# Performance work log

Hardware: AMD Instinct MI355X
Metric: run time of the kernel (lower is better)

## Reference

```python
import jax, jax.numpy as jnp
import numpy as np

L, H, D_IN, D_OUT = 2, 768, 768, 512


def _gru_layer(x, w_ih, w_hh, b_ih, b_hh):
    # x: [B,T,D]; w_ih: [3H,D]; w_hh: [3H,H]; b_ih,b_hh: [3H]
    # PyTorch GRU gate order: r, z, n
    gates_x = jnp.einsum('btd,gd->btg', x, w_ih) + b_ih  # [B,T,3H], precomputed once
    gates_x = jnp.swapaxes(gates_x, 0, 1)  # [T,B,3H] for scan over time
    h0 = jnp.zeros((x.shape[0], w_hh.shape[1]), dtype=x.dtype)

    def step(h, gx):
        gh = h @ w_hh.T + b_hh  # [B,3H]
        xr, xz, xn = jnp.split(gx, 3, axis=-1)
        hr, hz, hn = jnp.split(gh, 3, axis=-1)
        r = jax.nn.sigmoid(xr + hr)
        z = jax.nn.sigmoid(xz + hz)
        n = jnp.tanh(xn + r * hn)
        h_new = (1.0 - z) * n + z * h
        return h_new, h_new

    _, ys = jax.lax.scan(step, h0, gates_x)  # ys: [T,B,H]
    return jnp.swapaxes(ys, 0, 1)  # [B,T,H]


def setup_inputs() -> dict:
    key = jax.random.key(0)
    ks = jax.random.split(key, 6)
    B, T = 16, 1024
    s = 1.0 / np.sqrt(H)  # PyTorch RNN init scale
    x = jax.random.normal(ks[0], (B, T, D_IN), dtype=jnp.float32)
    # stacked per-layer GRU weights (D_IN == H so layer 0 stacks cleanly)
    w_ih = jax.random.uniform(ks[1], (L, 3 * H, H), minval=-s, maxval=s, dtype=jnp.float32)
    w_hh = jax.random.uniform(ks[2], (L, 3 * H, H), minval=-s, maxval=s, dtype=jnp.float32)
    b_ih = jax.random.uniform(ks[3], (L, 3 * H), minval=-s, maxval=s, dtype=jnp.float32)
    b_hh = jax.random.uniform(ks[4], (L, 3 * H), minval=-s, maxval=s, dtype=jnp.float32)
    w_fc = jax.random.normal(ks[5], (D_OUT, H), dtype=jnp.float32) * 0.02
    b_fc = jnp.zeros((D_OUT,), dtype=jnp.float32)
    return {"x": x, "w_ih": w_ih, "w_hh": w_hh, "b_ih": b_ih, "b_hh": b_hh,
            "w_fc": w_fc, "b_fc": b_fc}


def reference(x, w_ih, w_hh, b_ih, b_hh, w_fc, b_fc):
    out = x
    for l in range(L):  # small fixed layer loop
        out = _gru_layer(out, w_ih[l], w_hh[l], b_ih[l], b_hh[l])
    out = jnp.einsum('bth,oh->bto', out, w_fc) + b_fc  # Linear(768->512)
    return jax.nn.gelu(out, approximate=False)  # torch gelu (exact)
```

## Files before the change

kernel.cpp:

```cpp
#include <hip/hip_runtime.h>
#include <hip/hip_bf16.h>

#define H     768
#define G3    2304
#define BATCH 16
#define TLEN  1024
#define DOUT  512
#define SLICE 32
#define WPG   24
#define NWG   96
#define NTHR  384

typedef __attribute__((ext_vector_type(8))) short short8;
typedef __attribute__((ext_vector_type(4))) float f32x4;
typedef __attribute__((ext_vector_type(4))) unsigned int u32x4;

union U8 { short8 s; unsigned u[4]; unsigned long long q[2]; };

__device__ __forceinline__ float b2f(ushort u) {
  union { unsigned int ui; float f; } v; v.ui = ((unsigned int)u) << 16; return v.f;
}
__device__ __forceinline__ ushort f2b(float f) {
  union { float f; unsigned int ui; } v; v.f = f;
  unsigned int u = v.ui;
  return (ushort)((u + 0x7fffu + ((u >> 16) & 1u)) >> 16);
}

__device__ __forceinline__ unsigned long long agent_ld64(const void* p) {
  return __hip_atomic_load((const unsigned long long*)p, __ATOMIC_RELAXED, __HIP_MEMORY_SCOPE_AGENT);
}
__device__ __forceinline__ unsigned agent_ld32(const void* p) {
  return __hip_atomic_load((const unsigned*)p, __ATOMIC_RELAXED, __HIP_MEMORY_SCOPE_AGENT);
}
__device__ __forceinline__ void agent_st32(void* p, unsigned v) {
  __hip_atomic_store((unsigned*)p, v, __ATOMIC_RELAXED, __HIP_MEMORY_SCOPE_AGENT);
}
__device__ __forceinline__ void agent_st64(void* p, unsigned long long v) {
  __hip_atomic_store((unsigned long long*)p, v, __ATOMIC_RELAXED, __HIP_MEMORY_SCOPE_AGENT);
}

__device__ __forceinline__ void ld64B_agent(const void* p, u32x4* r) {
  asm volatile(
    "global_load_dwordx4 %0, %4, off sc0 sc1\n\t"
    "global_load_dwordx4 %1, %4, off offset:16 sc0 sc1\n\t"
    "global_load_dwordx4 %2, %4, off offset:32 sc0 sc1\n\t"
    "global_load_dwordx4 %3, %4, off offset:48 sc0 sc1\n\t"
    "s_waitcnt vmcnt(0)"
    : "=&v"(r[0]), "=&v"(r[1]), "=&v"(r[2]), "=&v"(r[3])
    : "v"(p) : "memory");
}

__device__ __forceinline__ short8 loadA8(const void* base, bool bf, size_t eidx) {
  if (bf) return *(const short8*)((const ushort*)base + eidx);
  const uint4* f = (const uint4*)((const float*)base + eidx);
  uint4 lo = f[0];
  uint4 hi = f[1];
  U8 r;
  r.u[0] = __builtin_amdgcn_perm(lo.y, lo.x, 0x07060302);
  r.u[1] = __builtin_amdgcn_perm(lo.w, lo.z, 0x07060302);
  r.u[2] = __builtin_amdgcn_perm(hi.y, hi.x, 0x07060302);
  r.u[3] = __builtin_amdgcn_perm(hi.w, hi.z, 0x07060302);
  return r.s;
}
__device__ __forceinline__ short8 loadW8(const void* base, bool bf, size_t eidx) {
  if (bf) return *(const short8*)((const ushort*)base + eidx);
  const float* f = (const float*)base + eidx;
  short8 r;
  #pragma unroll
  for (int i = 0; i < 8; i++) r[i] = (short)f2b(f[i]);
  return r;
}
__device__ __forceinline__ float loadS(const void* p, bool bf, size_t i) {
  return bf ? b2f(((const ushort*)p)[i]) : ((const float*)p)[i];
}

__device__ __forceinline__ bool detect_bf16(const unsigned* xw, int tid, int nthr, int* sh) {
  if (tid == 0) *sh = 0;
  __syncthreads();
  int c = 0;
  for (int i = tid; i < 4096; i += nthr) {
    int e = (int)((xw[i] >> 7) & 0xFF);
    c += (e >= 110 && e <= 140) ? 1 : 0;
  }
  atomicAdd(sh, c);
  __syncthreads();
  return *sh > 2048;
}

__device__ __forceinline__ unsigned* flagp(unsigned* flags, int grp, int wgi, int rep) {
  return flags + (((grp * WPG + wgi) * 4 + rep) * 32);
}

__global__ __launch_bounds__(NTHR) void scan_kernel(
    const void* __restrict__ x,
    const void* __restrict__ w_ih,
    const void* __restrict__ w_hh,
    const void* __restrict__ b_ih,
    const void* __restrict__ b_hh,
    unsigned int* flags,
    unsigned int* dflag,
    ushort* h1buf,
    float*  gxbuf1,
    float*  gxbuf2,
    ushort* y2)
{
  const int wg   = blockIdx.x;
  const int grp  = wg / WPG;
  const int wgi  = wg % WPG;
  const int tid  = threadIdx.x;
  const int wave = tid >> 6;
  const int lane = tid & 63;
  const int quad = lane >> 4;
  const bool isL = (grp == 1 || grp == 3);

  __shared__ ushort h_lds[BATCH * H];
  __shared__ float ghs[96 * 17];
  __shared__ float hold[BATCH * SLICE];
  __shared__ float bih_s[96], bhh_s[96];
  __shared__ int   detsh;

  const bool isbf = detect_bf16((const unsigned*)x, tid, NTHR, &detsh);
  if (tid == 0) dflag[0] = isbf ? 1u : 0u;

  for (int i = tid; i < BATCH * SLICE; i += NTHR) hold[i] = 0.0f;

  if (isL) {
    size_t boff = (grp == 3) ? (size_t)G3 : 0;
    for (int gf = tid; gf < 96; gf += NTHR) {
      size_t gidx = boff + (size_t)(gf >> 5) * H + wgi * SLICE + (gf & 31);
      bih_s[gf] = loadS(b_ih, isbf, gidx);
      bhh_s[gf] = loadS(b_hh, isbf, gidx);
    }
  }

  const unsigned* pollp = nullptr;
  int polloff = 0;
  if (wave == 0) {
    if (grp == 0) {
      if (lane == 0) { pollp = flagp(flags, 1, wgi, 2); polloff = -2; }
    } else if (grp == 1) {
      if      (lane == 0)  { pollp = flagp(flags, 0, wgi, 0);       polloff = 0;  }
      else if (lane <= 24) { pollp = flagp(flags, 1, lane - 1, 0);  polloff = 0;  }
      else if (lane <= 48) { pollp = flagp(flags, 2, lane - 25, 0); polloff = -2; }
    } else if (grp == 2) {
      if      (lane < 24)  { pollp = flagp(flags, 1, lane, 1);      polloff = 0;  }
      else if (lane == 24) { pollp = flagp(flags, 3, wgi, 1);       polloff = -1; }
    } else {
      if      (lane == 0)  { pollp = flagp(flags, 2, wgi, 1);       polloff = -1; }
      else if (lane <= 24) { pollp = flagp(flags, 3, lane - 1, 0);  polloff = 0;  }
    }
  }

  const void* Wmat = (grp == 0 || grp == 2) ? w_ih : w_hh;
  const size_t woff = (grp >= 2) ? (size_t)G3 * H : 0;
  const int gate   = wave >> 1;
  const int gfbase = gate * SLICE + (wave & 1) * 16;
  const int nrow   = gate * H + wgi * SLICE + (wave & 1) * 16 + (lane & 15);
  const size_t wbase = woff + (size_t)nrow * H + quad * 8;

  short8 bfrag[24];
  #pragma unroll
  for (int kk = 0; kk < 24; kk++)
    bfrag[kk] = loadW8(Wmat, isbf, wbase + kk * 32);

  const int sb  = tid / 24;
  const int seg = tid % 24;
  const int sx  = sb & 7;

  const int pb = tid >> 4;
  const int pj = (tid & 15) * 2;
  const bool pact = isL && (tid < BATCH * SLICE / 2);

  const int lag = (grp == 1) ? 1 : ((grp == 2) ? 2 : ((grp == 3) ? 4 : 0));

  __syncthreads();

  for (int t = 0; t < TLEN + 4; t++) {
    const int tau = t - lag;
    const bool active = (tau >= 0) && (tau < TLEN);

    if (active) {
      if (wave == 0) {
        for (;;) {
          int v = pollp ? (int)agent_ld32(pollp) : 0x7FFFFFFF;
          if (__ballot(v < t + polloff) == 0ull) break;
          __builtin_amdgcn_s_sleep(1);
        }
      }
      __syncthreads();

      unsigned long long gr01 = 0, gz01 = 0, gn01 = 0;
      if (pact) {
        const float* gxr = ((grp == 1) ? gxbuf1 : gxbuf2)
            + ((size_t)((tau & 3) * WPG + wgi) * BATCH + pb) * 96;
        gr01 = agent_ld64(gxr + pj);
        gz01 = agent_ld64(gxr + 32 + pj);
        gn01 = agent_ld64(gxr + 64 + pj);
      }

      if (grp == 0) {
        const size_t srcbase = ((size_t)sb * TLEN + tau) * H + seg * 32;
        #pragma unroll
        for (int i = 0; i < 4; i++) {
          short8 v = loadA8(x, isbf, srcbase + i * 8);
          *(short8*)&h_lds[sb * H + (((seg * 4 + i) ^ sx) * 8)] = v;
        }
      } else {
        const int hstep = (grp == 3) ? (t - 5) : (t - 2);
        u32x4 r4[4];
        if (hstep >= 0) {
          const ushort* src = (grp == 3)
              ? y2 + ((size_t)sb * TLEN + hstep) * H + seg * 32
              : h1buf + (size_t)(hstep & 3) * (BATCH * H) + (size_t)sb * H + seg * 32;
          ld64B_agent(src, r4);
        } else {
          r4[0] = (u32x4){0u, 0u, 0u, 0u};
          r4[1] = r4[0]; r4[2] = r4[0]; r4[3] = r4[0];
        }
        #pragma unroll
        for (int j = 0; j < 4; j++)
          *(u32x4*)&h_lds[sb * H + (((seg * 4 + j) ^ sx) * 8)] = r4[j];
      }
      __syncthreads();

      const int ar  = lane & 15;
      const int arx = ar & 7;
      const ushort* abase = &h_lds[ar * H];
      f32x4 acc0 = {0.f, 0.f, 0.f, 0.f}, acc1 = {0.f, 0.f, 0.f, 0.f};
      #pragma unroll
      for (int kk = 0; kk < 12; kk++) {
        short8 a0 = *(const short8*)&abase[((quad + 4 * kk) ^ arx) * 8];
        short8 a1 = *(const short8*)&abase[((quad + 4 * (kk + 12)) ^ arx) * 8];
        acc0 = __builtin_amdgcn_mfma_f32_16x16x32_bf16(a0, bfrag[kk],      acc0, 0, 0, 0);
        acc1 = __builtin_amdgcn_mfma_f32_16x16x32_bf16(a1, bfrag[kk + 12], acc1, 0, 0, 0);
      }
      f32x4 acc = acc0 + acc1;

      #pragma unroll
      for (int i = 0; i < 4; i++)
        ghs[(gfbase + (lane & 15)) * 17 + quad * 4 + i] = acc[i];
      __syncthreads();

      if (!isL) {
        float* gxout = ((grp == 0) ? gxbuf1 : gxbuf2)
            + ((size_t)(tau & 3) * WPG + wgi) * BATCH * 96;
        const int m  = tid / 24;
        const int c4 = (tid % 24) * 4;
        union { unsigned long long q; float f[2]; } p0, p1;
        p0.f[0] = ghs[(c4 + 0) * 17 + m];
        p0.f[1] = ghs[(c4 + 1) * 17 + m];
        p1.f[0] = ghs[(c4 + 2) * 17 + m];
        p1.f[1] = ghs[(c4 + 3) * 17 + m];
        agent_st64(gxout + (size_t)m * 96 + c4,     p0.q);
        agent_st64(gxout + (size_t)m * 96 + c4 + 2, p1.q);
      } else if (pact) {
        union { unsigned long long q; float f[2]; } ur, uz, un;
        ur.q = gr01; uz.q = gz01; un.q = gn01;
        unsigned hpack = 0;
        #pragma unroll
        for (int s = 0; s < 2; s++) {
          const int j = pj + s;
          float rpre = ur.f[s] + bih_s[j]      + ghs[j * 17 + pb]        + bhh_s[j];
          float zpre = uz.f[s] + bih_s[32 + j] + ghs[(32 + j) * 17 + pb] + bhh_s[32 + j];
          float hn   = ghs[(64 + j) * 17 + pb] + bhh_s[64 + j];
          float r = 1.0f / (1.0f + expf(-rpre));
          float z = 1.0f / (1.0f + expf(-zpre));
          float n = tanhf(un.f[s] + bih_s[64 + j] + r * hn);
          float hnew = (1.0f - z) * n + z * hold[pb * SLICE + j];
          hold[pb * SLICE + j] = hnew;
          hpack |= ((unsigned)f2b(hnew)) << (16 * s);
        }
        if (grp == 1)
          agent_st32(h1buf + (size_t)(tau & 3) * (BATCH * H)
                           + (size_t)pb * H + wgi * SLICE + pj, hpack);
        else
          agent_st32(&y2[((size_t)pb * TLEN + tau) * H + wgi * SLICE + pj], hpack);
      }
    }

    __syncthreads();
    if (tid < 4) agent_st32(flagp(flags, grp, wgi, tid), (unsigned)(t + 1));
  }
}

__global__ __launch_bounds__(256) void fc_kernel(
    const ushort* __restrict__ y2,
    const void* __restrict__ w_fc,
    const void* __restrict__ b_fc,
    const unsigned* __restrict__ dflag,
    void* __restrict__ out)
{
  const bool isbf = dflag[0] != 0u;
  const int wave = threadIdx.x >> 6;
  const int lane = threadIdx.x & 63;
  const int col  = lane & 15;
  const int quad = lane >> 4;
  const int m0 = blockIdx.x * 64 + wave * 16;
  const int n0 = blockIdx.y * 64;

  const ushort* arow = y2 + (size_t)(m0 + col) * H + quad * 8;
  const size_t bbase = (size_t)(n0 + col) * H + quad * 8;

  f32x4 acc[4];
  #pragma unroll
  for (int nt = 0; nt < 4; nt++) acc[nt] = (f32x4){0.f, 0.f, 0.f, 0.f};

  for (int kk = 0; kk < 24; kk++) {
    short8 a = *(const short8*)(arow + kk * 32);
    #pragma unroll
    for (int nt = 0; nt < 4; nt++) {
      short8 b = loadA8(w_fc, isbf, bbase + (size_t)nt * 16 * H + kk * 32);
      acc[nt] = __builtin_amdgcn_mfma_f32_16x16x32_bf16(a, b, acc[nt], 0, 0, 0);
    }
  }

  #pragma unroll
  for (int nt = 0; nt < 4; nt++) {
    #pragma unroll
    for (int i = 0; i < 4; i++) {
      int m = m0 + quad * 4 + i;
      int n = n0 + nt * 16 + col;
      float v = acc[nt][i] + loadS(b_fc, isbf, n);
      float g = 0.5f * v * (1.0f + erff(v * 0.70710678118654752f));
      if (isbf) ((ushort*)out)[(size_t)m * DOUT + n] = f2b(g);
      else      ((float*)out)[(size_t)m * DOUT + n] = g;
    }
  }
}

extern "C" void kernel_launch(void* const* d_in, const int* in_sizes, int n_in,
                              void* d_out, int out_size, void* d_ws, size_t ws_size,
                              hipStream_t stream) {
  const void* x    = d_in[0];
  const void* w_ih = d_in[1];
  const void* w_hh = d_in[2];
  const void* b_ih = d_in[3];
  const void* b_hh = d_in[4];
  const void* w_fc = d_in[5];
  const void* b_fc = d_in[6];

  char* ws = (char*)d_ws;
  unsigned int* flags = (unsigned int*)(ws);
  unsigned int* dflag = (unsigned int*)(ws + 49152);
  ushort* h1buf  = (ushort*)(ws + 53248);
  float*  gxbuf1 = (float*)(ws + 151552);
  float*  gxbuf2 = (float*)(ws + 741376);
  ushort* y2     = (ushort*)(ws + 1331200);

  hipMemsetAsync(ws, 0, 49156, stream);
  scan_kernel<<<dim3(NWG), dim3(NTHR), 0, stream>>>(
      x, w_ih, w_hh, b_ih, b_hh, flags, dflag,
      h1buf, gxbuf1, gxbuf2, y2);
  fc_kernel<<<dim3(16384 / 64, DOUT / 64), dim3(256), 0, stream>>>(
      y2, w_fc, b_fc, dflag, (void*)d_out);
}
```

Measured before the change: 3.676 ms.

## Merge layer-2 input projection into layer-1 recurrent group, cutting workgroups to 72

```diff
diff --git a/kernel.cpp b/kernel.cpp
--- a/kernel.cpp
+++ b/kernel.cpp
@@ -8,7 +8,7 @@
 #define DOUT  512
 #define SLICE 32
 #define WPG   24
-#define NWG   96
+#define NWG   72
 #define NTHR  384
 
 typedef __attribute__((ext_vector_type(8))) short short8;
@@ -48,6 +48,13 @@
     "s_waitcnt vmcnt(0)"
     : "=&v"(r[0]), "=&v"(r[1]), "=&v"(r[2]), "=&v"(r[3])
     : "v"(p) : "memory");
+}
+
+__device__ __forceinline__ float fsigmoid(float x) {
+  return 1.0f / (1.0f + __expf(-x));
+}
+__device__ __forceinline__ float ftanh(float x) {
+  return 1.0f - 2.0f / (__expf(2.0f * x) + 1.0f);
 }
 
 __device__ __forceinline__ short8 loadA8(const void* base, bool bf, size_t eidx) {
@@ -91,7 +98,7 @@
   return flags + (((grp * WPG + wgi) * 4 + rep) * 32);
 }
 
-__global__ __launch_bounds__(NTHR) void scan_kernel(
+__global__ __launch_bounds__(NTHR, 1) void scan_kernel(
     const void* __restrict__ x,
     const void* __restrict__ w_ih,
     const void* __restrict__ w_hh,
@@ -111,10 +118,10 @@
   const int wave = tid >> 6;
   const int lane = tid & 63;
   const int quad = lane >> 4;
-  const bool isL = (grp == 1 || grp == 3);
 
   __shared__ ushort h_lds[BATCH * H];
   __shared__ float ghs[96 * 17];
+  __shared__ float ghs2[96 * 17];
   __shared__ float hold[BATCH * SLICE];
   __shared__ float bih_s[96], bhh_s[96];
   __shared__ int   detsh;
@@ -124,8 +131,8 @@
 
   for (int i = tid; i < BATCH * SLICE; i += NTHR) hold[i] = 0.0f;
 
-  if (isL) {
-    size_t boff = (grp == 3) ? (size_t)G3 : 0;
+  if (grp >= 1) {
+    size_t boff = (grp == 2) ? (size_t)G3 : 0;
     for (int gf = tid; gf < 96; gf += NTHR) {
       size_t gidx = boff + (size_t)(gf >> 5) * H + wgi * SLICE + (gf & 31);
       bih_s[gf] = loadS(b_ih, isbf, gidx);
@@ -139,29 +146,33 @@
     if (grp == 0) {
       if (lane == 0) { pollp = flagp(flags, 1, wgi, 2); polloff = -2; }
     } else if (grp == 1) {
-      if      (lane == 0)  { pollp = flagp(flags, 0, wgi, 0);       polloff = 0;  }
-      else if (lane <= 24) { pollp = flagp(flags, 1, lane - 1, 0);  polloff = 0;  }
-      else if (lane <= 48) { pollp = flagp(flags, 2, lane - 25, 0); polloff = -2; }
-    } else if (grp == 2) {
-      if      (lane < 24)  { pollp = flagp(flags, 1, lane, 1);      polloff = 0;  }
-      else if (lane == 24) { pollp = flagp(flags, 3, wgi, 1);       polloff = -1; }
+      if      (lane == 0)  { pollp = flagp(flags, 0, wgi, 0);      polloff = 0;  }
+      else if (lane <= 24) { pollp = flagp(flags, 1, lane - 1, 0); polloff = 0;  }
+      else if (lane == 25) { pollp = flagp(flags, 2, wgi, 1);      polloff = -1; }
     } else {
-      if      (lane == 0)  { pollp = flagp(flags, 2, wgi, 1);       polloff = -1; }
-      else if (lane <= 24) { pollp = flagp(flags, 3, lane - 1, 0);  polloff = 0;  }
+      if      (lane == 0)  { pollp = flagp(flags, 1, wgi, 1);      polloff = -1; }
+      else if (lane <= 24) { pollp = flagp(flags, 2, lane - 1, 0); polloff = 0;  }
     }
   }
 
-  const void* Wmat = (grp == 0 || grp == 2) ? w_ih : w_hh;
-  const size_t woff = (grp >= 2) ? (size_t)G3 * H : 0;
+  const void* WmatA = (grp == 0) ? w_ih : w_hh;
+  const size_t woffA = (grp == 2) ? (size_t)G3 * H : 0;
   const int gate   = wave >> 1;
   const int gfbase = gate * SLICE + (wave & 1) * 16;
   const int nrow   = gate * H + wgi * SLICE + (wave & 1) * 16 + (lane & 15);
-  const size_t wbase = woff + (size_t)nrow * H + quad * 8;
+  const size_t wrow = (size_t)nrow * H + quad * 8;
 
   short8 bfrag[24];
   #pragma unroll
   for (int kk = 0; kk < 24; kk++)
-    bfrag[kk] = loadW8(Wmat, isbf, wbase + kk * 32);
+    bfrag[kk] = loadW8(WmatA, isbf, woffA + wrow + kk * 32);
+
+  short8 bfrag2[24];
+  if (grp == 1) {
+    #pragma unroll
+    for (int kk = 0; kk < 24; kk++)
+      bfrag2[kk] = loadW8(w_ih, isbf, (size_t)G3 * H + wrow + kk * 32);
+  }
 
   const int sb  = tid / 24;
   const int seg = tid % 24;
@@ -169,15 +180,17 @@
 
   const int pb = tid >> 4;
   const int pj = (tid & 15) * 2;
-  const bool pact = isL && (tid < BATCH * SLICE / 2);
-
-  const int lag = (grp == 1) ? 1 : ((grp == 2) ? 2 : ((grp == 3) ? 4 : 0));
+  const bool pact = (grp >= 1) && (tid < BATCH * SLICE / 2);
+
+  const int lag = (grp == 1) ? 1 : ((grp == 2) ? 4 : 0);
 
   __syncthreads();
 
   for (int t = 0; t < TLEN + 4; t++) {
     const int tau = t - lag;
-    const bool active = (tau >= 0) && (tau < TLEN);
+    const bool act_h = (tau >= 0) && (tau < TLEN);
+    const bool act_g = (grp == 1) && (t >= 2) && (t - 2 < TLEN);
+    const bool active = act_h || act_g;
 
     if (active) {
       if (wave == 0) {
@@ -190,7 +203,7 @@
       __syncthreads();
 
       unsigned long long gr01 = 0, gz01 = 0, gn01 = 0;
-      if (pact) {
+      if (pact && act_h) {
         const float* gxr = ((grp == 1) ? gxbuf1 : gxbuf2)
             + ((size_t)((tau & 3) * WPG + wgi) * BATCH + pb) * 96;
         gr01 = agent_ld64(gxr + pj);
@@ -206,10 +219,10 @@
           *(short8*)&h_lds[sb * H + (((seg * 4 + i) ^ sx) * 8)] = v;
         }
       } else {
-        const int hstep = (grp == 3) ? (t - 5) : (t - 2);
+        const int hstep = (grp == 1) ? (t - 2) : (t - 5);
         u32x4 r4[4];
         if (hstep >= 0) {
-          const ushort* src = (grp == 3)
+          const ushort* src = (grp == 2)
               ? y2 + ((size_t)sb * TLEN + hstep) * H + seg * 32
               : h1buf + (size_t)(hstep & 3) * (BATCH * H) + (size_t)sb * H + seg * 32;
           ld64B_agent(src, r4);
@@ -227,23 +240,41 @@
       const int arx = ar & 7;
       const ushort* abase = &h_lds[ar * H];
       f32x4 acc0 = {0.f, 0.f, 0.f, 0.f}, acc1 = {0.f, 0.f, 0.f, 0.f};
-      #pragma unroll
-      for (int kk = 0; kk < 12; kk++) {
-        short8 a0 = *(const short8*)&abase[((quad + 4 * kk) ^ arx) * 8];
-        short8 a1 = *(const short8*)&abase[((quad + 4 * (kk + 12)) ^ arx) * 8];
-        acc0 = __builtin_amdgcn_mfma_f32_16x16x32_bf16(a0, bfrag[kk],      acc0, 0, 0, 0);
-        acc1 = __builtin_amdgcn_mfma_f32_16x16x32_bf16(a1, bfrag[kk + 12], acc1, 0, 0, 0);
-      }
-      f32x4 acc = acc0 + acc1;
+      f32x4 acc2 = {0.f, 0.f, 0.f, 0.f}, acc3 = {0.f, 0.f, 0.f, 0.f};
+      if (grp == 1) {
+        #pragma unroll
+        for (int kk = 0; kk < 12; kk++) {
+          short8 a0 = *(const short8*)&abase[((quad + 4 * kk) ^ arx) * 8];
+          short8 a1 = *(const short8*)&abase[((quad + 4 * (kk + 12)) ^ arx) * 8];
+          acc0 = __builtin_amdgcn_mfma_f32_16x16x32_bf16(a0, bfrag[kk],       acc0, 0, 0, 0);
+          acc1 = __builtin_amdgcn_mfma_f32_16x16x32_bf16(a1, bfrag[kk + 12],  acc1, 0, 0, 0);
+          acc2 = __builtin_amdgcn_mfma_f32_16x16x32_bf16(a0, bfrag2[kk],      acc2, 0, 0, 0);
+          acc3 = __builtin_amdgcn_mfma_f32_16x16x32_bf16(a1, bfrag2[kk + 12], acc3, 0, 0, 0);
+        }
+      } else {
+        #pragma unroll
+        for (int kk = 0; kk < 12; kk++) {
+          short8 a0 = *(const short8*)&abase[((quad + 4 * kk) ^ arx) * 8];
+          short8 a1 = *(const short8*)&abase[((quad + 4 * (kk + 12)) ^ arx) * 8];
+          acc0 = __builtin_amdgcn_mfma_f32_16x16x32_bf16(a0, bfrag[kk],      acc0, 0, 0, 0);
+          acc1 = __builtin_amdgcn_mfma_f32_16x16x32_bf16(a1, bfrag[kk + 12], acc1, 0, 0, 0);
+        }
+      }
+      f32x4 accA = acc0 + acc1;
 
       #pragma unroll
       for (int i = 0; i < 4; i++)
-        ghs[(gfbase + (lane & 15)) * 17 + quad * 4 + i] = acc[i];
+        ghs[(gfbase + ar) * 17 + quad * 4 + i] = accA[i];
+      if (grp == 1) {
+        f32x4 accB = acc2 + acc3;
+        #pragma unroll
+        for (int i = 0; i < 4; i++)
+          ghs2[(gfbase + ar) * 17 + quad * 4 + i] = accB[i];
+      }
       __syncthreads();
 
-      if (!isL) {
-        float* gxout = ((grp == 0) ? gxbuf1 : gxbuf2)
-            + ((size_t)(tau & 3) * WPG + wgi) * BATCH * 96;
+      if (grp == 0) {
+        float* gxout = gxbuf1 + ((size_t)(tau & 3) * WPG + wgi) * BATCH * 96;
         const int m  = tid / 24;
         const int c4 = (tid % 24) * 4;
         union { unsigned long long q; float f[2]; } p0, p1;
@@ -253,33 +284,47 @@
         p1.f[1] = ghs[(c4 + 3) * 17 + m];
         agent_st64(gxout + (size_t)m * 96 + c4,     p0.q);
         agent_st64(gxout + (size_t)m * 96 + c4 + 2, p1.q);
-      } else if (pact) {
-        union { unsigned long long q; float f[2]; } ur, uz, un;
-        ur.q = gr01; uz.q = gz01; un.q = gn01;
-        unsigned hpack = 0;
-        #pragma unroll
-        for (int s = 0; s < 2; s++) {
-          const int j = pj + s;
-          float rpre = ur.f[s] + bih_s[j]      + ghs[j * 17 + pb]        + bhh_s[j];
-          float zpre = uz.f[s] + bih_s[32 + j] + ghs[(32 + j) * 17 + pb] + bhh_s[32 + j];
-          float hn   = ghs[(64 + j) * 17 + pb] + bhh_s[64 + j];
-          float r = 1.0f / (1.0f + expf(-rpre));
-          float z = 1.0f / (1.0f + expf(-zpre));
-          float n = tanhf(un.f[s] + bih_s[64 + j] + r * hn);
-          float hnew = (1.0f - z) * n + z * hold[pb * SLICE + j];
-          hold[pb * SLICE + j] = hnew;
-          hpack |= ((unsigned)f2b(hnew)) << (16 * s);
-        }
-        if (grp == 1)
-          agent_st32(h1buf + (size_t)(tau & 3) * (BATCH * H)
-                           + (size_t)pb * H + wgi * SLICE + pj, hpack);
-        else
-          agent_st32(&y2[((size_t)pb * TLEN + tau) * H + wgi * SLICE + pj], hpack);
+      } else {
+        if (act_g) {
+          float* gxout = gxbuf2 + ((size_t)((t - 2) & 3) * WPG + wgi) * BATCH * 96;
+          const int m  = tid / 24;
+          const int c4 = (tid % 24) * 4;
+          union { unsigned long long q; float f[2]; } p0, p1;
+          p0.f[0] = ghs2[(c4 + 0) * 17 + m];
+          p0.f[1] = ghs2[(c4 + 1) * 17 + m];
+          p1.f[0] = ghs2[(c4 + 2) * 17 + m];
+          p1.f[1] = ghs2[(c4 + 3) * 17 + m];
+          agent_st64(gxout + (size_t)m * 96 + c4,     p0.q);
+          agent_st64(gxout + (size_t)m * 96 + c4 + 2, p1.q);
+        }
+        if (act_h && pact) {
+          union { unsigned long long q; float f[2]; } ur, uz, un;
+          ur.q = gr01; uz.q = gz01; un.q = gn01;
+          unsigned hpack = 0;
+          #pragma unroll
+          for (int s = 0; s < 2; s++) {
+            const int j = pj + s;
+            float rpre = ur.f[s] + bih_s[j]      + ghs[j * 17 + pb]        + bhh_s[j];
+            float zpre = uz.f[s] + bih_s[32 + j] + ghs[(32 + j) * 17 + pb] + bhh_s[32 + j];
+            float hn   = ghs[(64 + j) * 17 + pb] + bhh_s[64 + j];
+            float r = fsigmoid(rpre);
+            float z = fsigmoid(zpre);
+            float n = ftanh(un.f[s] + bih_s[64 + j] + r * hn);
+            float hnew = (1.0f - z) * n + z * hold[pb * SLICE + j];
+            hold[pb * SLICE + j] = hnew;
+            hpack |= ((unsigned)f2b(hnew)) << (16 * s);
+          }
+          if (grp == 1)
+            agent_st32(h1buf + (size_t)(tau & 3) * (BATCH * H)
+                             + (size_t)pb * H + wgi * SLICE + pj, hpack);
+          else
+            agent_st32(&y2[((size_t)pb * TLEN + tau) * H + wgi * SLICE + pj], hpack);
+        }
       }
     }
 
     __syncthreads();
-    if (tid < 4) agent_st32(flagp(flags, grp, wgi, tid), (unsigned)(t + 1));
+    if (tid < 3) agent_st32(flagp(flags, grp, wgi, tid), (unsigned)(t + 1));
   }
 }
 
```

Result: slower. 5.007 ms (+36.2%).

## Halve scan workgroup count by widening each workgroup to 64 gate columns

Applied to the files above, without the earlier changes.

```diff
diff --git a/kernel.cpp b/kernel.cpp
--- a/kernel.cpp
+++ b/kernel.cpp
@@ -6,10 +6,10 @@
 #define BATCH 16
 #define TLEN  1024
 #define DOUT  512
-#define SLICE 32
-#define WPG   24
-#define NWG   96
-#define NTHR  384
+#define GCOL  64
+#define WPG   12
+#define NWG   48
+#define NTHR  768
 
 typedef __attribute__((ext_vector_type(8))) short short8;
 typedef __attribute__((ext_vector_type(4))) float f32x4;
@@ -39,14 +39,12 @@
   __hip_atomic_store((unsigned long long*)p, v, __ATOMIC_RELAXED, __HIP_MEMORY_SCOPE_AGENT);
 }
 
-__device__ __forceinline__ void ld64B_agent(const void* p, u32x4* r) {
+__device__ __forceinline__ void ld32B_agent(const void* p, u32x4* r) {
   asm volatile(
-    "global_load_dwordx4 %0, %4, off sc0 sc1\n\t"
-    "global_load_dwordx4 %1, %4, off offset:16 sc0 sc1\n\t"
-    "global_load_dwordx4 %2, %4, off offset:32 sc0 sc1\n\t"
-    "global_load_dwordx4 %3, %4, off offset:48 sc0 sc1\n\t"
+    "global_load_dwordx4 %0, %2, off sc0 sc1\n\t"
+    "global_load_dwordx4 %1, %2, off offset:16 sc0 sc1\n\t"
     "s_waitcnt vmcnt(0)"
-    : "=&v"(r[0]), "=&v"(r[1]), "=&v"(r[2]), "=&v"(r[3])
+    : "=&v"(r[0]), "=&v"(r[1])
     : "v"(p) : "memory");
 }
 
@@ -114,20 +112,20 @@
   const bool isL = (grp == 1 || grp == 3);
 
   __shared__ ushort h_lds[BATCH * H];
-  __shared__ float ghs[96 * 17];
-  __shared__ float hold[BATCH * SLICE];
-  __shared__ float bih_s[96], bhh_s[96];
+  __shared__ float ghs[192 * 17];
+  __shared__ float hold[BATCH * GCOL];
+  __shared__ float bih_s[192], bhh_s[192];
   __shared__ int   detsh;
 
   const bool isbf = detect_bf16((const unsigned*)x, tid, NTHR, &detsh);
   if (tid == 0) dflag[0] = isbf ? 1u : 0u;
 
-  for (int i = tid; i < BATCH * SLICE; i += NTHR) hold[i] = 0.0f;
+  for (int i = tid; i < BATCH * GCOL; i += NTHR) hold[i] = 0.0f;
 
   if (isL) {
     size_t boff = (grp == 3) ? (size_t)G3 : 0;
-    for (int gf = tid; gf < 96; gf += NTHR) {
-      size_t gidx = boff + (size_t)(gf >> 5) * H + wgi * SLICE + (gf & 31);
+    for (int gf = tid; gf < 192; gf += NTHR) {
+      size_t gidx = boff + (size_t)(gf >> 6) * H + wgi * GCOL + (gf & 63);
       bih_s[gf] = loadS(b_ih, isbf, gidx);
       bhh_s[gf] = loadS(b_hh, isbf, gidx);
     }
@@ -140,22 +138,23 @@
       if (lane == 0) { pollp = flagp(flags, 1, wgi, 2); polloff = -2; }
     } else if (grp == 1) {
       if      (lane == 0)  { pollp = flagp(flags, 0, wgi, 0);       polloff = 0;  }
-      else if (lane <= 24) { pollp = flagp(flags, 1, lane - 1, 0);  polloff = 0;  }
-      else if (lane <= 48) { pollp = flagp(flags, 2, lane - 25, 0); polloff = -2; }
+      else if (lane <= 12) { pollp = flagp(flags, 1, lane - 1, 0);  polloff = 0;  }
+      else if (lane <= 24) { pollp = flagp(flags, 2, lane - 13, 0); polloff = -2; }
     } else if (grp == 2) {
-      if      (lane < 24)  { pollp = flagp(flags, 1, lane, 1);      polloff = 0;  }
-      else if (lane == 24) { pollp = flagp(flags, 3, wgi, 1);       polloff = -1; }
+      if      (lane < 12)  { pollp = flagp(flags, 1, lane, 1);      polloff = 0;  }
+      else if (lane == 12) { pollp = flagp(flags, 3, wgi, 1);       polloff = -1; }
     } else {
       if      (lane == 0)  { pollp = flagp(flags, 2, wgi, 1);       polloff = -1; }
-      else if (lane <= 24) { pollp = flagp(flags, 3, lane - 1, 0);  polloff = 0;  }
+      else if (lane <= 12) { pollp = flagp(flags, 3, lane - 1, 0);  polloff = 0;  }
     }
   }
 
   const void* Wmat = (grp == 0 || grp == 2) ? w_ih : w_hh;
   const size_t woff = (grp >= 2) ? (size_t)G3 * H : 0;
-  const int gate   = wave >> 1;
-  const int gfbase = gate * SLICE + (wave & 1) * 16;
-  const int nrow   = gate * H + wgi * SLICE + (wave & 1) * 16 + (lane & 15);
+  const int gate   = wave >> 2;
+  const int wchunk = wave & 3;
+  const int gfbase = gate * GCOL + wchunk * 16;
+  const int nrow   = gate * H + wgi * GCOL + wchunk * 16 + (lane & 15);
   const size_t wbase = woff + (size_t)nrow * H + quad * 8;
 
   short8 bfrag[24];
@@ -163,13 +162,13 @@
   for (int kk = 0; kk < 24; kk++)
     bfrag[kk] = loadW8(Wmat, isbf, wbase + kk * 32);
 
-  const int sb  = tid / 24;
-  const int seg = tid % 24;
+  const int sb  = tid / 48;
+  const int seg = tid % 48;
   const int sx  = sb & 7;
 
-  const int pb = tid >> 4;
-  const int pj = (tid & 15) * 2;
-  const bool pact = isL && (tid < BATCH * SLICE / 2);
+  const int pb = tid >> 5;
+  const int pj = (tid & 31) * 2;
+  const bool pact = isL && (tid < BATCH * GCOL / 2);
 
   const int lag = (grp == 1) ? 1 : ((grp == 2) ? 2 : ((grp == 3) ? 4 : 0));
 
@@ -192,34 +191,34 @@
       unsigned long long gr01 = 0, gz01 = 0, gn01 = 0;
       if (pact) {
         const float* gxr = ((grp == 1) ? gxbuf1 : gxbuf2)
-            + ((size_t)((tau & 3) * WPG + wgi) * BATCH + pb) * 96;
+            + ((size_t)((tau & 3) * WPG + wgi) * BATCH + pb) * 192;
         gr01 = agent_ld64(gxr + pj);
-        gz01 = agent_ld64(gxr + 32 + pj);
-        gn01 = agent_ld64(gxr + 64 + pj);
+        gz01 = agent_ld64(gxr + 64 + pj);
+        gn01 = agent_ld64(gxr + 128 + pj);
       }
 
       if (grp == 0) {
-        const size_t srcbase = ((size_t)sb * TLEN + tau) * H + seg * 32;
-        #pragma unroll
-        for (int i = 0; i < 4; i++) {
-          short8 v = loadA8(x, isbf, srcbase + i * 8);
-          *(short8*)&h_lds[sb * H + (((seg * 4 + i) ^ sx) * 8)] = v;
-        }
+        const size_t srcbase = ((size_t)sb * TLEN + tau) * H + seg * 16;
+        short8 v0 = loadA8(x, isbf, srcbase);
+        short8 v1 = loadA8(x, isbf, srcbase + 8);
+        const int u0 = seg * 2, u1 = seg * 2 + 1;
+        *(short8*)&h_lds[sb * H + (((u0 & ~7) | ((u0 & 7) ^ sx)) * 8)] = v0;
+        *(short8*)&h_lds[sb * H + (((u1 & ~7) | ((u1 & 7) ^ sx)) * 8)] = v1;
       } else {
         const int hstep = (grp == 3) ? (t - 5) : (t - 2);
-        u32x4 r4[4];
+        u32x4 r4[2];
         if (hstep >= 0) {
           const ushort* src = (grp == 3)
-              ? y2 + ((size_t)sb * TLEN + hstep) * H + seg * 32
-              : h1buf + (size_t)(hstep & 3) * (BATCH * H) + (size_t)sb * H + seg * 32;
-          ld64B_agent(src, r4);
+              ? y2 + ((size_t)sb * TLEN + hstep) * H + seg * 16
+              : h1buf + (size_t)(hstep & 3) * (BATCH * H) + (size_t)sb * H + seg * 16;
+          ld32B_agent(src, r4);
         } else {
           r4[0] = (u32x4){0u, 0u, 0u, 0u};
-          r4[1] = r4[0]; r4[2] = r4[0]; r4[3] = r4[0];
+          r4[1] = r4[0];
         }
-        #pragma unroll
-        for (int j = 0; j < 4; j++)
-          *(u32x4*)&h_lds[sb * H + (((seg * 4 + j) ^ sx) * 8)] = r4[j];
+        const int u0 = seg * 2, u1 = seg * 2 + 1;
+        *(u32x4*)&h_lds[sb * H + (((u0 & ~7) | ((u0 & 7) ^ sx)) * 8)] = r4[0];
+        *(u32x4*)&h_lds[sb * H + (((u1 & ~7) | ((u1 & 7) ^ sx)) * 8)] = r4[1];
       }
       __syncthreads();
 
@@ -229,8 +228,10 @@
       f32x4 acc0 = {0.f, 0.f, 0.f, 0.f}, acc1 = {0.f, 0.f, 0.f, 0.f};
       #pragma unroll
       for (int kk = 0; kk < 12; kk++) {
-        short8 a0 = *(const short8*)&abase[((quad + 4 * kk) ^ arx) * 8];
-        short8 a1 = *(const short8*)&abase[((quad + 4 * (kk + 12)) ^ arx) * 8];
+        const int ua = quad + 4 * kk;
+        const int ub = quad + 4 * (kk + 12);
+        short8 a0 = *(const short8*)&abase[(((ua & ~7) | ((ua & 7) ^ arx)) * 8)];
+        short8 a1 = *(const short8*)&abase[(((ub & ~7) | ((ub & 7) ^ arx)) * 8)];
         acc0 = __builtin_amdgcn_mfma_f32_16x16x32_bf16(a0, bfrag[kk],      acc0, 0, 0, 0);
         acc1 = __builtin_amdgcn_mfma_f32_16x16x32_bf16(a1, bfrag[kk + 12], acc1, 0, 0, 0);
       }
@@ -238,21 +239,21 @@
 
       #pragma unroll
       for (int i = 0; i < 4; i++)
-        ghs[(gfbase + (lane & 15)) * 17 + quad * 4 + i] = acc[i];
+        ghs[(gfbase + ar) * 17 + quad * 4 + i] = acc[i];
       __syncthreads();
 
       if (!isL) {
         float* gxout = ((grp == 0) ? gxbuf1 : gxbuf2)
-            + ((size_t)(tau & 3) * WPG + wgi) * BATCH * 96;
-        const int m  = tid / 24;
-        const int c4 = (tid % 24) * 4;
+            + ((size_t)(tau & 3) * WPG + wgi) * BATCH * 192;
+        const int m  = tid / 48;
+        const int c4 = (tid % 48) * 4;
         union { unsigned long long q; float f[2]; } p0, p1;
         p0.f[0] = ghs[(c4 + 0) * 17 + m];
         p0.f[1] = ghs[(c4 + 1) * 17 + m];
         p1.f[0] = ghs[(c4 + 2) * 17 + m];
         p1.f[1] = ghs[(c4 + 3) * 17 + m];
-        agent_st64(gxout + (size_t)m * 96 + c4,     p0.q);
-        agent_st64(gxout + (size_t)m * 96 + c4 + 2, p1.q);
+        agent_st64(gxout + (size_t)m * 192 + c4,     p0.q);
+        agent_st64(gxout + (size_t)m * 192 + c4 + 2, p1.q);
       } else if (pact) {
         union { unsigned long long q; float f[2]; } ur, uz, un;
         ur.q = gr01; uz.q = gz01; un.q = gn01;
@@ -260,26 +261,26 @@
         #pragma unroll
         for (int s = 0; s < 2; s++) {
           const int j = pj + s;
-          float rpre = ur.f[s] + bih_s[j]      + ghs[j * 17 + pb]        + bhh_s[j];
-          float zpre = uz.f[s] + bih_s[32 + j] + ghs[(32 + j) * 17 + pb] + bhh_s[32 + j];
-          float hn   = ghs[(64 + j) * 17 + pb] + bhh_s[64 + j];
+          float rpre = ur.f[s] + bih_s[j]       + ghs[j * 17 + pb]         + bhh_s[j];
+          float zpre = uz.f[s] + bih_s[64 + j]  + ghs[(64 + j) * 17 + pb]  + bhh_s[64 + j];
+          float hn   = ghs[(128 + j) * 17 + pb] + bhh_s[128 + j];
           float r = 1.0f / (1.0f + expf(-rpre));
           float z = 1.0f / (1.0f + expf(-zpre));
-          float n = tanhf(un.f[s] + bih_s[64 + j] + r * hn);
-          float hnew = (1.0f - z) * n + z * hold[pb * SLICE + j];
-          hold[pb * SLICE + j] = hnew;
+          float n = tanhf(un.f[s] + bih_s[128 + j] + r * hn);
+          float hnew = (1.0f - z) * n + z * hold[pb * GCOL + j];
+          hold[pb * GCOL + j] = hnew;
           hpack |= ((unsigned)f2b(hnew)) << (16 * s);
         }
         if (grp == 1)
           agent_st32(h1buf + (size_t)(tau & 3) * (BATCH * H)
-                           + (size_t)pb * H + wgi * SLICE + pj, hpack);
+                           + (size_t)pb * H + wgi * GCOL + pj, hpack);
         else
-          agent_st32(&y2[((size_t)pb * TLEN + tau) * H + wgi * SLICE + pj], hpack);
+          agent_st32(&y2[((size_t)pb * TLEN + tau) * H + wgi * GCOL + pj], hpack);
       }
     }
 
     __syncthreads();
-    if (tid < 4) agent_st32(flagp(flags, grp, wgi, tid), (unsigned)(t + 1));
+    if (tid < 3) agent_st32(flagp(flags, grp, wgi, tid), (unsigned)(t + 1));
   }
 }
 
@@ -341,13 +342,13 @@
 
   char* ws = (char*)d_ws;
   unsigned int* flags = (unsigned int*)(ws);
-  unsigned int* dflag = (unsigned int*)(ws + 49152);
-  ushort* h1buf  = (ushort*)(ws + 53248);
-  float*  gxbuf1 = (float*)(ws + 151552);
-  float*  gxbuf2 = (float*)(ws + 741376);
-  ushort* y2     = (ushort*)(ws + 1331200);
-
-  hipMemsetAsync(ws, 0, 49156, stream);
+  unsigned int* dflag = (unsigned int*)(ws + 24576);
+  ushort* h1buf  = (ushort*)(ws + 28672);
+  float*  gxbuf1 = (float*)(ws + 126976);
+  float*  gxbuf2 = (float*)(ws + 716800);
+  ushort* y2     = (ushort*)(ws + 1306624);
+
+  hipMemsetAsync(ws, 0, 24580, stream);
   scan_kernel<<<dim3(NWG), dim3(NTHR), 0, stream>>>(
       x, w_ih, w_hh, b_ih, b_hh, flags, dflag,
       h1buf, gxbuf1, gxbuf2, y2);
```

Result: slower. 4.134 ms (+12.5%).

## Fuse FC+GELU into persistent scan kernel with flag-polled consumer workgroups

Applied to the files above, without the earlier changes.

```diff
diff --git a/kernel.cpp b/kernel.cpp
--- a/kernel.cpp
+++ b/kernel.cpp
@@ -8,7 +8,9 @@
 #define DOUT  512
 #define SLICE 32
 #define WPG   24
-#define NWG   96
+#define NSCAN 96
+#define NFC   64
+#define NWG   160
 #define NTHR  384
 
 typedef __attribute__((ext_vector_type(8))) short short8;
@@ -97,21 +99,20 @@
     const void* __restrict__ w_hh,
     const void* __restrict__ b_ih,
     const void* __restrict__ b_hh,
+    const void* __restrict__ w_fc,
+    const void* __restrict__ b_fc,
     unsigned int* flags,
-    unsigned int* dflag,
     ushort* h1buf,
     float*  gxbuf1,
     float*  gxbuf2,
-    ushort* y2)
+    ushort* y2,
+    void* __restrict__ out)
 {
   const int wg   = blockIdx.x;
-  const int grp  = wg / WPG;
-  const int wgi  = wg % WPG;
   const int tid  = threadIdx.x;
   const int wave = tid >> 6;
   const int lane = tid & 63;
   const int quad = lane >> 4;
-  const bool isL = (grp == 1 || grp == 3);
 
   __shared__ ushort h_lds[BATCH * H];
   __shared__ float ghs[96 * 17];
@@ -120,7 +121,78 @@
   __shared__ int   detsh;
 
   const bool isbf = detect_bf16((const unsigned*)x, tid, NTHR, &detsh);
-  if (tid == 0) dflag[0] = isbf ? 1u : 0u;
+
+  if (wg >= NSCAN) {
+    const int fcw = wg - NSCAN;
+    const unsigned* fpoll = (wave == 0 && lane < WPG)
+        ? flagp(flags, 3, lane, (fcw < 32) ? 2 : 3) : nullptr;
+    const int sb  = tid / 24;
+    const int seg = tid % 24;
+    const int sx  = sb & 7;
+    const int ar  = lane & 15;
+    const int arx = ar & 7;
+
+    for (int i = 0; i < 16; i++) {
+      const int t = fcw + 64 * i;
+      if (wave == 0) {
+        const int tgt = t + 5;
+        for (;;) {
+          int v = fpoll ? (int)agent_ld32(fpoll) : 0x7FFFFFFF;
+          if (__ballot(v < tgt) == 0ull) break;
+          __builtin_amdgcn_s_sleep(8);
+        }
+      }
+      __syncthreads();
+
+      {
+        const ushort* src = y2 + ((size_t)sb * TLEN + t) * H + seg * 32;
+        u32x4 r4[4];
+        ld64B_agent(src, r4);
+        #pragma unroll
+        for (int j = 0; j < 4; j++)
+          *(u32x4*)&h_lds[sb * H + (((seg * 4 + j) ^ sx) * 8)] = r4[j];
+      }
+      __syncthreads();
+
+      if (wave < 4) {
+        const int n0 = wave * 128;
+        const ushort* abase = &h_lds[ar * H];
+        f32x4 acc[8];
+        #pragma unroll
+        for (int nt = 0; nt < 8; nt++) acc[nt] = (f32x4){0.f, 0.f, 0.f, 0.f};
+        for (int kk = 0; kk < 12; kk++) {
+          short8 a0 = *(const short8*)&abase[((quad + 4 * kk) ^ arx) * 8];
+          short8 a1 = *(const short8*)&abase[((quad + 4 * (kk + 12)) ^ arx) * 8];
+          #pragma unroll
+          for (int nt = 0; nt < 8; nt++) {
+            const size_t bb = (size_t)(n0 + nt * 16 + ar) * H + quad * 8;
+            short8 b0 = loadA8(w_fc, isbf, bb + kk * 32);
+            short8 b1 = loadA8(w_fc, isbf, bb + (kk + 12) * 32);
+            acc[nt] = __builtin_amdgcn_mfma_f32_16x16x32_bf16(a0, b0, acc[nt], 0, 0, 0);
+            acc[nt] = __builtin_amdgcn_mfma_f32_16x16x32_bf16(a1, b1, acc[nt], 0, 0, 0);
+          }
+        }
+        #pragma unroll
+        for (int nt = 0; nt < 8; nt++) {
+          #pragma unroll
+          for (int i2 = 0; i2 < 4; i2++) {
+            const int b = quad * 4 + i2;
+            const int n = n0 + nt * 16 + ar;
+            float v = acc[nt][i2] + loadS(b_fc, isbf, n);
+            float g = 0.5f * v * (1.0f + erff(v * 0.70710678118654752f));
+            if (isbf) ((ushort*)out)[((size_t)b * TLEN + t) * DOUT + n] = f2b(g);
+            else      ((float*)out)[((size_t)b * TLEN + t) * DOUT + n] = g;
+          }
+        }
+      }
+      __syncthreads();
+    }
+    return;
+  }
+
+  const int grp  = wg / WPG;
+  const int wgi  = wg % WPG;
+  const bool isL = (grp == 1 || grp == 3);
 
   for (int i = tid; i < BATCH * SLICE; i += NTHR) hold[i] = 0.0f;
 
@@ -238,7 +310,7 @@
 
       #pragma unroll
       for (int i = 0; i < 4; i++)
-        ghs[(gfbase + (lane & 15)) * 17 + quad * 4 + i] = acc[i];
+        ghs[(gfbase + ar) * 17 + quad * 4 + i] = acc[i];
       __syncthreads();
 
       if (!isL) {
@@ -283,51 +355,6 @@
   }
 }
 
-__global__ __launch_bounds__(256) void fc_kernel(
-    const ushort* __restrict__ y2,
-    const void* __restrict__ w_fc,
-    const void* __restrict__ b_fc,
-    const unsigned* __restrict__ dflag,
-    void* __restrict__ out)
-{
-  const bool isbf = dflag[0] != 0u;
-  const int wave = threadIdx.x >> 6;
-  const int lane = threadIdx.x & 63;
-  const int col  = lane & 15;
-  const int quad = lane >> 4;
-  const int m0 = blockIdx.x * 64 + wave * 16;
-  const int n0 = blockIdx.y * 64;
-
-  const ushort* arow = y2 + (size_t)(m0 + col) * H + quad * 8;
-  const size_t bbase = (size_t)(n0 + col) * H + quad * 8;
-
-  f32x4 acc[4];
-  #pragma unroll
-  for (int nt = 0; nt < 4; nt++) acc[nt] = (f32x4){0.f, 0.f, 0.f, 0.f};
-
-  for (int kk = 0; kk < 24; kk++) {
-    short8 a = *(const short8*)(arow + kk * 32);
-    #pragma unroll
-    for (int nt = 0; nt < 4; nt++) {
-      short8 b = loadA8(w_fc, isbf, bbase + (size_t)nt * 16 * H + kk * 32);
-      acc[nt] = __builtin_amdgcn_mfma_f32_16x16x32_bf16(a, b, acc[nt], 0, 0, 0);
-    }
-  }
-
-  #pragma unroll
-  for (int nt = 0; nt < 4; nt++) {
-    #pragma unroll
-    for (int i = 0; i < 4; i++) {
-      int m = m0 + quad * 4 + i;
-      int n = n0 + nt * 16 + col;
-      float v = acc[nt][i] + loadS(b_fc, isbf, n);
-      float g = 0.5f * v * (1.0f + erff(v * 0.70710678118654752f));
-      if (isbf) ((ushort*)out)[(size_t)m * DOUT + n] = f2b(g);
-      else      ((float*)out)[(size_t)m * DOUT + n] = g;
-    }
-  }
-}
-
 extern "C" void kernel_launch(void* const* d_in, const int* in_sizes, int n_in,
                               void* d_out, int out_size, void* d_ws, size_t ws_size,
                               hipStream_t stream) {
@@ -341,16 +368,13 @@
 
   char* ws = (char*)d_ws;
   unsigned int* flags = (unsigned int*)(ws);
-  unsigned int* dflag = (unsigned int*)(ws + 49152);
   ushort* h1buf  = (ushort*)(ws + 53248);
   float*  gxbuf1 = (float*)(ws + 151552);
   float*  gxbuf2 = (float*)(ws + 741376);
   ushort* y2     = (ushort*)(ws + 1331200);
 
-  hipMemsetAsync(ws, 0, 49156, stream);
+  hipMemsetAsync(ws, 0, 49152, stream);
   scan_kernel<<<dim3(NWG), dim3(NTHR), 0, stream>>>(
-      x, w_ih, w_hh, b_ih, b_hh, flags, dflag,
-      h1buf, gxbuf1, gxbuf2, y2);
-  fc_kernel<<<dim3(16384 / 64, DOUT / 64), dim3(256), 0, stream>>>(
-      y2, w_fc, b_fc, dflag, (void*)d_out);
-}
+      x, w_ih, w_hh, b_ih, b_hh, w_fc, b_fc, flags,
+      h1buf, gxbuf1, gxbuf2, y2, d_out);
+}
```

Result: faster. 3.553 ms (-3.3%).
